# Kernel tuning notes

Hardware: AMD Instinct MI355X
Metric: run time of the kernel (lower is better)

Reference implementation:

```python
import jax, jax.numpy as jnp
import numpy as np

F = 64          # n_features
H = F * F       # n_hidden = 4096
P = 4           # proj_size
T = 8192        # timesteps


def _proj_lstm_cell_zero_state(x, W_ih, W_hh, b_ih, b_hh, W_hr):
    """One PyTorch proj-LSTM layer applied per-timestep with zero initial
    (h, c). x: [T, in_dim] -> [T, P].  With h0=0, W_hh contributes 0 and
    f*c_prev vanishes."""
    h0 = jnp.zeros((x.shape[0], W_hh.shape[1]), x.dtype)
    gates = x @ W_ih.T + h0 @ W_hh.T + b_ih + b_hh          # [T, 4H]
    i, f, g, o = jnp.split(gates, 4, axis=-1)               # PyTorch gate order
    c = jax.nn.sigmoid(i) * jnp.tanh(g)                     # f*c0 = 0
    h = jax.nn.sigmoid(o) * jnp.tanh(c)                     # [T, H]
    return h @ W_hr.T                                       # [T, P]


def setup_inputs() -> dict:
    key = jax.random.key(0)
    ks = jax.random.split(key, 17)
    s = 0.05
    d = {"x": jax.random.normal(ks[0], (T, F), jnp.float32)}
    shapes = {
        "W_ih_0": (4 * H, F), "W_hh_0": (4 * H, P), "b_ih_0": (4 * H,),
        "b_hh_0": (4 * H,), "W_hr_0": (P, H),
        "W_ih_1": (4 * H, P), "W_hh_1": (4 * H, P), "b_ih_1": (4 * H,),
        "b_hh_1": (4 * H,), "W_hr_1": (P, H),
        "W_ih_2": (4 * H, P), "W_hh_2": (4 * H, P), "b_ih_2": (4 * H,),
        "b_hh_2": (4 * H,), "W_hr_2": (P, H),
    }
    for i, (name, shp) in enumerate(shapes.items()):
        d[name] = s * jax.random.normal(ks[i + 1], shp, jnp.float32)
    return d


def reference(x,
              W_ih_0, W_hh_0, b_ih_0, b_hh_0, W_hr_0,
              W_ih_1, W_hh_1, b_ih_1, b_hh_1, W_hr_1,
              W_ih_2, W_hh_2, b_ih_2, b_hh_2, W_hr_2):
    # study(): inputs.split(1, dim=0) feeds each timestep as a fresh length-1
    # sequence with zero initial state, so timesteps are independent ->
    # vectorize over T instead of the per-step Python loop.
    h = _proj_lstm_cell_zero_state(x, W_ih_0, W_hh_0, b_ih_0, b_hh_0, W_hr_0)
    h = _proj_lstm_cell_zero_state(h, W_ih_1, W_hh_1, b_ih_1, b_hh_1, W_hr_1)
    h = _proj_lstm_cell_zero_state(h, W_ih_2, W_hh_2, b_ih_2, b_hh_2, W_hr_2)
    return h  # [T, P]
```

## Files before the change

### kernel.cpp

```cpp
#include <hip/hip_runtime.h>

#define TSTEPS 8192
#define HDIM 4096
#define PDIM 4
#define KDIM 64

typedef unsigned short u16;
typedef __attribute__((ext_vector_type(8))) short short8;
typedef __attribute__((ext_vector_type(4))) float f32x4;

#define S1 -1.44269504089f
#define S2 -2.88539008177f

#if __has_builtin(__builtin_amdgcn_exp2f)
#define EXP2(x) __builtin_amdgcn_exp2f(x)
#else
#define EXP2(x) exp2f(x)
#endif
__device__ __forceinline__ float rcpf(float x) { return __builtin_amdgcn_rcpf(x); }

__device__ __forceinline__ float h_merge(float c, float ec) {
  float c2 = c * c;
  float num = c * fmaf(c2, 10.0f, 105.0f);
  float den = fmaf(c2, 45.0f, 105.0f) + c2 * c2;
  return num * rcpf(den * (1.0f + ec));
}

__device__ __forceinline__ float sig_poly(float z) {
  float z2 = z * z;
  float q = fmaf(z2, -2.1081349e-4f, 2.0833333e-3f);
  q = fmaf(z2, q, -2.0833333e-2f);
  q = fmaf(z2, q, 0.25f);
  return fmaf(z, q, 0.5f);
}
__device__ __forceinline__ float tanh_poly(float z) {
  float z2 = z * z;
  float q = fmaf(z2, -5.3968254e-2f, 1.3333333e-1f);
  q = fmaf(z2, q, -3.3333333e-1f);
  q = fmaf(z2, q, 1.0f);
  return z * q;
}

__device__ __forceinline__ void gload16(const void* g, void* l) {
  __builtin_amdgcn_global_load_lds((const __attribute__((address_space(1))) unsigned int*)g,
                                   (__attribute__((address_space(3))) unsigned int*)l,
                                   16, 0, 0);
}

__device__ __forceinline__ u16 bf16_rne(float f) {
  unsigned u = __float_as_uint(f);
  u += 0x7FFF + ((u >> 16) & 1);
  return (u16)(u >> 16);
}
__device__ __forceinline__ void hilo(float v, u16& h, u16& l) {
  h = bf16_rne(v);
  l = bf16_rne(v - __uint_as_float((unsigned)h << 16));
}

#define WS_Y0   0
#define WS_Y1   32768
#define WS_BSC  65536
#define WS_C1   77824
#define WS_C2   159744
#define WS_XHI  241664
#define WS_XLO  503808
#define WS_WHI  765952
#define WS_WLO  1159168
#define WS_PP   1552384
#define WS_BP   3649536

__global__ void prep_kernel(const float* __restrict__ x,
                            const float* __restrict__ Wih0, const float* __restrict__ bih0,
                            const float* __restrict__ bhh0,
                            const float* __restrict__ Wih1, const float* __restrict__ bih1,
                            const float* __restrict__ bhh1, const float* __restrict__ Whr1,
                            const float* __restrict__ Wih2, const float* __restrict__ bih2,
                            const float* __restrict__ bhh2, const float* __restrict__ Whr2,
                            float* __restrict__ ws) {
  const int i = blockIdx.x * 256 + threadIdx.x;
  u16* xhi = (u16*)(ws + WS_XHI);
  u16* xlo = (u16*)(ws + WS_XLO);
  u16* whi = (u16*)(ws + WS_WHI);
  u16* wlo = (u16*)(ws + WS_WLO);

  if (i < 131072) {
    float4 v = *(const float4*)&x[i * 4];
    float val[4] = {v.x, v.y, v.z, v.w};
    u16 h[4], l[4];
#pragma unroll
    for (int e = 0; e < 4; ++e) hilo(val[e], h[e], l[e]);
    *(ushort4*)&xhi[i * 4] = make_ushort4(h[0], h[1], h[2], h[3]);
    *(ushort4*)&xlo[i * 4] = make_ushort4(l[0], l[1], l[2], l[3]);
  } else if (i < 327680) {
    int f = i - 131072;
    int el4 = f * 4;
    int r = el4 >> 6;
    int k4 = el4 & 63;
    int gate = r >> 12, jr = r & 4095;
    int src = (gate == 0) ? jr : (gate + 1) * HDIM + jr;
    float sc = (gate == 1) ? S2 : S1;
    float4 v = *(const float4*)&Wih0[(size_t)src * KDIM + k4];
    float val[4] = {sc * v.x, sc * v.y, sc * v.z, sc * v.w};
    u16 h[4], l[4];
#pragma unroll
    for (int e = 0; e < 4; ++e) hilo(val[e], h[e], l[e]);
    *(ushort4*)&whi[r * KDIM + k4] = make_ushort4(h[0], h[1], h[2], h[3]);
    *(ushort4*)&wlo[r * KDIM + k4] = make_ushort4(l[0], l[1], l[2], l[3]);
  } else if (i < 339968) {
    int f = i - 327680;
    int g = f >> 12, j = f & 4095;
    int src = (g == 0) ? j : (g + 1) * HDIM + j;
    float sc = (g == 1) ? S2 : S1;
    ws[WS_BSC + f] = sc * (bih0[src] + bhh0[src]);
  } else if (i < 348160) {
    int f = i - 339968;
    const float* Wih = (f < 4096) ? Wih1 : Wih2;
    const float* bih = (f < 4096) ? bih1 : bih2;
    const float* bhh = (f < 4096) ? bhh1 : bhh2;
    const float* Whr = (f < 4096) ? Whr1 : Whr2;
    float* c = ws + ((f < 4096) ? WS_C1 : WS_C2);
    int j = f & 4095;
    *(float4*)(c + j * 4)         = *(const float4*)&Wih[(size_t)j * 4];
    *(float4*)(c + 16384 + j * 4) = *(const float4*)&Wih[(size_t)(2 * HDIM + j) * 4];
    *(float4*)(c + 32768 + j * 4) = *(const float4*)&Wih[(size_t)(3 * HDIM + j) * 4];
    *(float4*)(c + 49152 + j * 4) = make_float4(bih[j] + bhh[j],
                                      bih[2 * HDIM + j] + bhh[2 * HDIM + j],
                                      bih[3 * HDIM + j] + bhh[3 * HDIM + j], 0.f);
    *(float4*)(c + 65536 + j * 4) = make_float4(Whr[j], Whr[HDIM + j], Whr[2 * HDIM + j], Whr[3 * HDIM + j]);
  } else if (i < 446464) {
    int f = i - 348160;
    int lane = f & 63;
    int tg = f >> 6;
    int L = tg / 768;
    int r2 = tg - L * 768;
    int g = r2 >> 8, tile = r2 & 255;
    const float* Wih = (L == 0) ? Wih1 : Wih2;
    const float* bih = (L == 0) ? bih1 : bih2;
    const float* bhh = (L == 0) ? bhh1 : bhh2;
    int q = lane >> 4, n = lane & 15;
    int j = tile * 16 + n;
    int go = (g == 0) ? 0 : (g + 1) * HDIM;
    u16 v[8] = {0, 0, 0, 0, 0, 0, 0, 0};
    if (q < 2) {
#pragma unroll
      for (int e = 0; e < 8; ++e) {
        float wv = Wih[(size_t)(go + j) * 4 + (e & 3)];
        u16 h, l;
        hilo(wv, h, l);
        v[e] = (q == 0) ? h : l;
      }
    } else if (q == 2) {
      float bv = bih[go + j] + bhh[go + j];
      hilo(bv, v[0], v[1]);
    }
    u16* bpp = (u16*)(ws + WS_BP);
    *(short8*)&bpp[(size_t)f * 8] =
        (short8){(short)v[0], (short)v[1], (short)v[2], (short)v[3],
                 (short)v[4], (short)v[5], (short)v[6], (short)v[7]};
  }
}

__global__ __launch_bounds__(256, 2)
void lstm_layer0_mfma(const u16* __restrict__ xhi, const u16* __restrict__ xlo,
                      const u16* __restrict__ whi, const u16* __restrict__ wlo,
                      const float* __restrict__ bsc, const float* __restrict__ Whr,
                      float* __restrict__ pp) {
  __shared__ __align__(16) char smem[65536];
  u16* lw_hi = (u16*)smem;
  u16* lw_lo = (u16*)(smem + 24576);
  u16* lx    = (u16*)(smem + 49152);

  const int tid = threadIdx.x;
  const int w = tid >> 6, lane = tid & 63;
  const int m = lane & 15, q = lane >> 4;
  const int jb = blockIdx.x & 63, tbb = blockIdx.x >> 6;
  const int j0 = jb * 64;
  const int t0 = tbb * 256;

  const int r8_ = lane >> 3;
  const int swo = ((lane & 7) ^ r8_) * 8;

#pragma unroll
  for (int ui = 0; ui < 16; ++ui) {
    const int u = w * 16 + ui;
    const u16* g;
    char* l;
    if (u < 24) {
      g = whi + (size_t)((u >> 3) * HDIM + j0 + (u & 7) * 8 + r8_) * 64 + swo;
      l = smem + u * 1024;
    } else if (u < 48) {
      int uu = u - 24;
      g = wlo + (size_t)((uu >> 3) * HDIM + j0 + (uu & 7) * 8 + r8_) * 64 + swo;
      l = smem + 24576 + uu * 1024;
    } else {
      int uu = u - 48;
      g = xhi + (size_t)(t0 + uu * 8 + r8_) * 64 + swo;
      l = smem + 49152 + uu * 1024;
    }
    gload16(g, l);
  }

  float whr_v[4][4];
#pragma unroll
  for (int p = 0; p < 4; ++p)
#pragma unroll
    for (int js = 0; js < 4; ++js)
      whr_v[p][js] = Whr[(size_t)p * HDIM + j0 + js * 16 + m];
  float biv[4], bgv[4], bov[4];
#pragma unroll
  for (int js = 0; js < 4; ++js) {
    const int j = j0 + js * 16 + m;
    biv[js] = bsc[j];
    bgv[js] = bsc[HDIM + j];
    bov[js] = bsc[2 * HDIM + j];
  }

  f32x4 acc[2][4][3];
  short8 al[2][2];

  auto zero_acc = [&]() {
#pragma unroll
    for (int ts = 0; ts < 2; ++ts)
#pragma unroll
      for (int js = 0; js < 4; ++js)
#pragma unroll
        for (int g = 0; g < 3; ++g) acc[ts][js][g] = (f32x4){0.f, 0.f, 0.f, 0.f};
  };
  auto load_al = [&](int tt) {
#pragma unroll
    for (int kc = 0; kc < 2; ++kc)
#pragma unroll
      for (int ts = 0; ts < 2; ++ts)
        al[kc][ts] = *(const short8*)&xlo[(size_t)(t0 + tt * 128 + w * 32 + ts * 16 + m) * KDIM + kc * 32 + q * 8];
  };
  auto compute = [&]() {
#pragma unroll
    for (int kc = 0; kc < 2; ++kc) {
      const int cs = ((kc * 4 + q) ^ (m & 7)) * 8;
      short8 ah[2];
#pragma unroll
      for (int ts = 0; ts < 2; ++ts)
        ah[ts] = *(const short8*)&lx[(w * 32 + ts * 16 + m) * 64 + cs];
#pragma unroll
      for (int js = 0; js < 4; ++js) {
#pragma unroll
        for (int g = 0; g < 3; ++g) {
          const int roff = (g * 64 + js * 16 + m) * 64 + cs;
          short8 bh = *(const short8*)&lw_hi[roff];
          short8 bl = *(const short8*)&lw_lo[roff];
#pragma unroll
          for (int ts = 0; ts < 2; ++ts) {
            acc[ts][js][g] = __builtin_amdgcn_mfma_f32_16x16x32_bf16(ah[ts], bh, acc[ts][js][g], 0, 0, 0);
            acc[ts][js][g] = __builtin_amdgcn_mfma_f32_16x16x32_bf16(al[kc][ts], bh, acc[ts][js][g], 0, 0, 0);
            acc[ts][js][g] = __builtin_amdgcn_mfma_f32_16x16x32_bf16(ah[ts], bl, acc[ts][js][g], 0, 0, 0);
          }
        }
      }
    }
  };
  auto act_proj = [&](int tt) {
    float hreg[2][4][4];
#pragma unroll
    for (int js = 0; js < 4; ++js) {
#pragma unroll
      for (int ts = 0; ts < 2; ++ts) {
#pragma unroll
        for (int r = 0; r < 4; ++r) {
          float ea = EXP2(acc[ts][js][0][r] + biv[js]);
          float eb = EXP2(acc[ts][js][1][r] + bgv[js]);
          float c = (1.0f - eb) * rcpf((1.0f + ea) * (1.0f + eb));
          float ec = EXP2(acc[ts][js][2][r] + bov[js]);
          hreg[ts][js][r] = h_merge(c, ec);
        }
      }
    }
#pragma unroll
    for (int ts = 0; ts < 2; ++ts) {
#pragma unroll
      for (int r = 0; r < 4; ++r) {
        float pv[4];
#pragma unroll
        for (int p = 0; p < 4; ++p) {
          float s = 0.f;
#pragma unroll
          for (int js = 0; js < 4; ++js) s = fmaf(hreg[ts][js][r], whr_v[p][js], s);
#pragma unroll
          for (int ofs = 1; ofs < 16; ofs <<= 1) s += __shfl_xor(s, ofs, 16);
          pv[p] = s;
        }
        if (m == 0) {
          const int t = t0 + tt * 128 + w * 32 + ts * 16 + q * 4 + r;
          *(float4*)&pp[((size_t)jb * TSTEPS + t) * PDIM] = make_float4(pv[0], pv[1], pv[2], pv[3]);
        }
      }
    }
  };

  load_al(0);
  zero_acc();
  __syncthreads();
  compute();
  __syncthreads();
#pragma unroll
  for (int ui = 0; ui < 4; ++ui) {
    const int u = w * 4 + ui;
    gload16(xhi + (size_t)(t0 + 128 + u * 8 + r8_) * 64 + swo, smem + 49152 + u * 1024);
  }
  load_al(1);
  act_proj(0);
  zero_acc();
  __syncthreads();
  compute();
  act_proj(1);
}

__global__ void fused_rest(const float* __restrict__ pp,
                           const float* __restrict__ c1, const float* __restrict__ c2,
                           const u16* __restrict__ bp,
                           float* __restrict__ out) {
  __shared__ float ytile[64];
  __shared__ float part[256];
  const int tid = threadIdx.x;
  const int t0 = blockIdx.x * 16;
  const int lane = tid & 63, w = tid >> 6;
  const int n = lane & 15, q = lane >> 4;

  {
    const int o = tid & 63;
    const int sg = tid >> 6;
    float s = 0.f;
#pragma unroll 4
    for (int k = sg * 16; k < sg * 16 + 16; ++k)
      s += pp[(size_t)k * (TSTEPS * PDIM) + t0 * PDIM + o];
    part[sg * 64 + o] = s;
  }
  __syncthreads();
  if (tid < 64) ytile[tid] = part[tid] + part[64 + tid] + part[128 + tid] + part[192 + tid];
  __syncthreads();

#pragma unroll
  for (int L = 0; L < 2; ++L) {
    const float4* cwr = (const float4*)(((L == 0) ? c1 : c2) + 65536);
    const u16* bL = bp + (size_t)L * 393216;

    float4 yv = *(const float4*)&ytile[n * 4];
    float ye[4] = {yv.x, yv.y, yv.z, yv.w};
    u16 yh[4], yl[4];
#pragma unroll
    for (int e = 0; e < 4; ++e) hilo(ye[e], yh[e], yl[e]);
    short8 af = (short8){0, 0, 0, 0, 0, 0, 0, 0};
    if (q < 2) {
      af[0] = (short)yh[0]; af[1] = (short)yh[1]; af[2] = (short)yh[2]; af[3] = (short)yh[3];
      af[4] = (short)yl[0]; af[5] = (short)yl[1]; af[6] = (short)yl[2]; af[7] = (short)yl[3];
    } else if (q == 2) {
      af[0] = (short)0x3F80;
      af[1] = (short)0x3F80;
    }

    float o_[4][4];
#pragma unroll
    for (int r = 0; r < 4; ++r)
#pragma unroll
      for (int p = 0; p < 4; ++p) o_[r][p] = 0.f;

#pragma unroll 2
    for (int jt = 0; jt < 64; ++jt) {
      const int tile = w * 64 + jt;
      short8 bfi = *(const short8*)&bL[((size_t)(0 * 256 + tile) * 64 + lane) * 8];
      short8 bfg = *(const short8*)&bL[((size_t)(1 * 256 + tile) * 64 + lane) * 8];
      short8 bfo = *(const short8*)&bL[((size_t)(2 * 256 + tile) * 64 + lane) * 8];
      const f32x4 zc = (f32x4){0.f, 0.f, 0.f, 0.f};
      f32x4 ai = __builtin_amdgcn_mfma_f32_16x16x32_bf16(af, bfi, zc, 0, 0, 0);
      f32x4 ag = __builtin_amdgcn_mfma_f32_16x16x32_bf16(af, bfg, zc, 0, 0, 0);
      f32x4 ao = __builtin_amdgcn_mfma_f32_16x16x32_bf16(af, bfo, zc, 0, 0, 0);
      float4 wr = cwr[tile * 16 + n];
#pragma unroll
      for (int r = 0; r < 4; ++r) {
        float cc = sig_poly(ai[r]) * tanh_poly(ag[r]);
        float h = tanh_poly(cc) * sig_poly(ao[r]);
        o_[r][0] = fmaf(h, wr.x, o_[r][0]);
        o_[r][1] = fmaf(h, wr.y, o_[r][1]);
        o_[r][2] = fmaf(h, wr.z, o_[r][2]);
        o_[r][3] = fmaf(h, wr.w, o_[r][3]);
      }
    }

#pragma unroll
    for (int r = 0; r < 4; ++r)
#pragma unroll
      for (int p = 0; p < 4; ++p) {
#pragma unroll
        for (int ofs = 1; ofs < 16; ofs <<= 1)
          o_[r][p] += __shfl_xor(o_[r][p], ofs, 16);
      }
    __syncthreads();
    if (n == 0) {
#pragma unroll
      for (int r = 0; r < 4; ++r)
#pragma unroll
        for (int p = 0; p < 4; ++p)
          part[w * 64 + (q * 4 + r) * 4 + p] = o_[r][p];
    }
    __syncthreads();
    if (tid < 64) ytile[tid] = part[tid] + part[64 + tid] + part[128 + tid] + part[192 + tid];
    __syncthreads();
  }

  if (tid < 64) out[t0 * PDIM + tid] = ytile[tid];
}

extern "C" void kernel_launch(void* const* d_in, const int* in_sizes, int n_in,
                              void* d_out, int out_size, void* d_ws, size_t ws_size,
                              hipStream_t stream) {
  const float* x    = (const float*)d_in[0];
  const float* Wih0 = (const float*)d_in[1];
  const float* bih0 = (const float*)d_in[3];
  const float* bhh0 = (const float*)d_in[4];
  const float* Whr0 = (const float*)d_in[5];
  const float* Wih1 = (const float*)d_in[6];
  const float* bih1 = (const float*)d_in[8];
  const float* bhh1 = (const float*)d_in[9];
  const float* Whr1 = (const float*)d_in[10];
  const float* Wih2 = (const float*)d_in[11];
  const float* bih2 = (const float*)d_in[13];
  const float* bhh2 = (const float*)d_in[14];
  const float* Whr2 = (const float*)d_in[15];
  float* out = (float*)d_out;
  float* ws = (float*)d_ws;
  float* pp = ws + WS_PP;

  prep_kernel<<<dim3(1744), dim3(256), 0, stream>>>(
      x, Wih0, bih0, bhh0, Wih1, bih1, bhh1, Whr1, Wih2, bih2, bhh2, Whr2, ws);

  lstm_layer0_mfma<<<dim3(2048), dim3(256), 0, stream>>>(
      (const u16*)(ws + WS_XHI), (const u16*)(ws + WS_XLO),
      (const u16*)(ws + WS_WHI), (const u16*)(ws + WS_WLO),
      ws + WS_BSC, Whr0, pp);

  fused_rest<<<dim3(512), dim3(256), 0, stream>>>(
      pp, ws + WS_C1, ws + WS_C2, (const u16*)(ws + WS_BP), out);
}
```

Before: 210.5 us.

## Load x fragments from global into registers and raise layer0 occupancy; widen fused_rest tiles

In layer 0, the x-hi tile is no longer staged in LDS. Its A fragments are loaded straight from global into registers, which cuts shared memory from 64KB to 48KB and lets launch bounds ask for 3 blocks per CU. The mid-kernel syncthreads barriers and LDS refill go away. The Whr load moves into the activation step to ease register pressure, at the cost of more register-held A operands and uncoalesced global reads. fused_rest now uses 512-thread blocks over 32 timesteps, so each weight fragment feeds two MFMA groups and weight traffic per block is halved.

```diff
diff --git a/kernel.cpp b/kernel.cpp
--- a/kernel.cpp
+++ b/kernel.cpp
@@ -160,15 +160,14 @@
   }
 }
 
-__global__ __launch_bounds__(256, 2)
+__global__ __launch_bounds__(256, 3)
 void lstm_layer0_mfma(const u16* __restrict__ xhi, const u16* __restrict__ xlo,
                       const u16* __restrict__ whi, const u16* __restrict__ wlo,
                       const float* __restrict__ bsc, const float* __restrict__ Whr,
                       float* __restrict__ pp) {
-  __shared__ __align__(16) char smem[65536];
+  __shared__ __align__(16) char smem[49152];
   u16* lw_hi = (u16*)smem;
   u16* lw_lo = (u16*)(smem + 24576);
-  u16* lx    = (u16*)(smem + 49152);
 
   const int tid = threadIdx.x;
   const int w = tid >> 6, lane = tid & 63;
@@ -181,31 +180,18 @@
   const int swo = ((lane & 7) ^ r8_) * 8;
 
 #pragma unroll
-  for (int ui = 0; ui < 16; ++ui) {
-    const int u = w * 16 + ui;
+  for (int ui = 0; ui < 12; ++ui) {
+    const int u = w * 12 + ui;
     const u16* g;
-    char* l;
     if (u < 24) {
       g = whi + (size_t)((u >> 3) * HDIM + j0 + (u & 7) * 8 + r8_) * 64 + swo;
-      l = smem + u * 1024;
-    } else if (u < 48) {
-      int uu = u - 24;
+    } else {
+      const int uu = u - 24;
       g = wlo + (size_t)((uu >> 3) * HDIM + j0 + (uu & 7) * 8 + r8_) * 64 + swo;
-      l = smem + 24576 + uu * 1024;
-    } else {
-      int uu = u - 48;
-      g = xhi + (size_t)(t0 + uu * 8 + r8_) * 64 + swo;
-      l = smem + 49152 + uu * 1024;
-    }
-    gload16(g, l);
+    }
+    gload16(g, smem + u * 1024);
   }
 
-  float whr_v[4][4];
-#pragma unroll
-  for (int p = 0; p < 4; ++p)
-#pragma unroll
-    for (int js = 0; js < 4; ++js)
-      whr_v[p][js] = Whr[(size_t)p * HDIM + j0 + js * 16 + m];
   float biv[4], bgv[4], bov[4];
 #pragma unroll
   for (int js = 0; js < 4; ++js) {
@@ -216,7 +202,7 @@
   }
 
   f32x4 acc[2][4][3];
-  short8 al[2][2];
+  short8 ah[2][2], al[2][2];
 
   auto zero_acc = [&]() {
 #pragma unroll
@@ -226,21 +212,20 @@
 #pragma unroll
         for (int g = 0; g < 3; ++g) acc[ts][js][g] = (f32x4){0.f, 0.f, 0.f, 0.f};
   };
-  auto load_al = [&](int tt) {
+  auto load_x = [&](int tt) {
 #pragma unroll
     for (int kc = 0; kc < 2; ++kc)
 #pragma unroll
-      for (int ts = 0; ts < 2; ++ts)
-        al[kc][ts] = *(const short8*)&xlo[(size_t)(t0 + tt * 128 + w * 32 + ts * 16 + m) * KDIM + kc * 32 + q * 8];
+      for (int ts = 0; ts < 2; ++ts) {
+        const size_t off = (size_t)(t0 + tt * 128 + w * 32 + ts * 16 + m) * KDIM + kc * 32 + q * 8;
+        ah[kc][ts] = *(const short8*)&xhi[off];
+        al[kc][ts] = *(const short8*)&xlo[off];
+      }
   };
   auto compute = [&]() {
 #pragma unroll
     for (int kc = 0; kc < 2; ++kc) {
       const int cs = ((kc * 4 + q) ^ (m & 7)) * 8;
-      short8 ah[2];
-#pragma unroll
-      for (int ts = 0; ts < 2; ++ts)
-        ah[ts] = *(const short8*)&lx[(w * 32 + ts * 16 + m) * 64 + cs];
 #pragma unroll
       for (int js = 0; js < 4; ++js) {
 #pragma unroll
@@ -250,32 +235,35 @@
           short8 bl = *(const short8*)&lw_lo[roff];
 #pragma unroll
           for (int ts = 0; ts < 2; ++ts) {
-            acc[ts][js][g] = __builtin_amdgcn_mfma_f32_16x16x32_bf16(ah[ts], bh, acc[ts][js][g], 0, 0, 0);
+            acc[ts][js][g] = __builtin_amdgcn_mfma_f32_16x16x32_bf16(ah[kc][ts], bh, acc[ts][js][g], 0, 0, 0);
             acc[ts][js][g] = __builtin_amdgcn_mfma_f32_16x16x32_bf16(al[kc][ts], bh, acc[ts][js][g], 0, 0, 0);
-            acc[ts][js][g] = __builtin_amdgcn_mfma_f32_16x16x32_bf16(ah[ts], bl, acc[ts][js][g], 0, 0, 0);
+            acc[ts][js][g] = __builtin_amdgcn_mfma_f32_16x16x32_bf16(ah[kc][ts], bl, acc[ts][js][g], 0, 0, 0);
           }
         }
       }
     }
   };
   auto act_proj = [&](int tt) {
-    float hreg[2][4][4];
-#pragma unroll
-    for (int js = 0; js < 4; ++js) {
-#pragma unroll
-      for (int ts = 0; ts < 2; ++ts) {
+    float whr_v[4][4];
+#pragma unroll
+    for (int p = 0; p < 4; ++p)
+#pragma unroll
+      for (int js = 0; js < 4; ++js)
+        whr_v[p][js] = Whr[(size_t)p * HDIM + j0 + js * 16 + m];
+#pragma unroll
+    for (int ts = 0; ts < 2; ++ts) {
+      float hreg[4][4];
+#pragma unroll
+      for (int js = 0; js < 4; ++js) {
 #pragma unroll
         for (int r = 0; r < 4; ++r) {
           float ea = EXP2(acc[ts][js][0][r] + biv[js]);
           float eb = EXP2(acc[ts][js][1][r] + bgv[js]);
           float c = (1.0f - eb) * rcpf((1.0f + ea) * (1.0f + eb));
           float ec = EXP2(acc[ts][js][2][r] + bov[js]);
-          hreg[ts][js][r] = h_merge(c, ec);
-        }
-      }
-    }
-#pragma unroll
-    for (int ts = 0; ts < 2; ++ts) {
+          hreg[js][r] = h_merge(c, ec);
+        }
+      }
 #pragma unroll
       for (int r = 0; r < 4; ++r) {
         float pv[4];
@@ -283,7 +271,7 @@
         for (int p = 0; p < 4; ++p) {
           float s = 0.f;
 #pragma unroll
-          for (int js = 0; js < 4; ++js) s = fmaf(hreg[ts][js][r], whr_v[p][js], s);
+          for (int js = 0; js < 4; ++js) s = fmaf(hreg[js][r], whr_v[p][js], s);
 #pragma unroll
           for (int ofs = 1; ofs < 16; ofs <<= 1) s += __shfl_xor(s, ofs, 16);
           pv[p] = s;
@@ -296,46 +284,42 @@
     }
   };
 
-  load_al(0);
+  load_x(0);
   zero_acc();
   __syncthreads();
   compute();
-  __syncthreads();
-#pragma unroll
-  for (int ui = 0; ui < 4; ++ui) {
-    const int u = w * 4 + ui;
-    gload16(xhi + (size_t)(t0 + 128 + u * 8 + r8_) * 64 + swo, smem + 49152 + u * 1024);
-  }
-  load_al(1);
   act_proj(0);
+  load_x(1);
   zero_acc();
-  __syncthreads();
   compute();
   act_proj(1);
 }
 
-__global__ void fused_rest(const float* __restrict__ pp,
-                           const float* __restrict__ c1, const float* __restrict__ c2,
-                           const u16* __restrict__ bp,
-                           float* __restrict__ out) {
-  __shared__ float ytile[64];
-  __shared__ float part[256];
+__global__ __launch_bounds__(512)
+void fused_rest(const float* __restrict__ pp,
+                const float* __restrict__ c1, const float* __restrict__ c2,
+                const u16* __restrict__ bp,
+                float* __restrict__ out) {
+  __shared__ float ytile[128];
+  __shared__ float part[512];
   const int tid = threadIdx.x;
-  const int t0 = blockIdx.x * 16;
+  const int t0 = blockIdx.x * 32;
   const int lane = tid & 63, w = tid >> 6;
   const int n = lane & 15, q = lane >> 4;
+  const int gt = w >> 2;
+  const int wj = w & 3;
 
   {
-    const int o = tid & 63;
-    const int sg = tid >> 6;
+    const int o = tid & 127;
+    const int sg = tid >> 7;
     float s = 0.f;
 #pragma unroll 4
     for (int k = sg * 16; k < sg * 16 + 16; ++k)
       s += pp[(size_t)k * (TSTEPS * PDIM) + t0 * PDIM + o];
-    part[sg * 64 + o] = s;
+    part[sg * 128 + o] = s;
   }
   __syncthreads();
-  if (tid < 64) ytile[tid] = part[tid] + part[64 + tid] + part[128 + tid] + part[192 + tid];
+  if (tid < 128) ytile[tid] = part[tid] + part[128 + tid] + part[256 + tid] + part[384 + tid];
   __syncthreads();
 
 #pragma unroll
@@ -343,70 +327,88 @@
     const float4* cwr = (const float4*)(((L == 0) ? c1 : c2) + 65536);
     const u16* bL = bp + (size_t)L * 393216;
 
-    float4 yv = *(const float4*)&ytile[n * 4];
-    float ye[4] = {yv.x, yv.y, yv.z, yv.w};
-    u16 yh[4], yl[4];
-#pragma unroll
-    for (int e = 0; e < 4; ++e) hilo(ye[e], yh[e], yl[e]);
-    short8 af = (short8){0, 0, 0, 0, 0, 0, 0, 0};
-    if (q < 2) {
-      af[0] = (short)yh[0]; af[1] = (short)yh[1]; af[2] = (short)yh[2]; af[3] = (short)yh[3];
-      af[4] = (short)yl[0]; af[5] = (short)yl[1]; af[6] = (short)yl[2]; af[7] = (short)yl[3];
-    } else if (q == 2) {
-      af[0] = (short)0x3F80;
-      af[1] = (short)0x3F80;
-    }
-
-    float o_[4][4];
-#pragma unroll
-    for (int r = 0; r < 4; ++r)
-#pragma unroll
-      for (int p = 0; p < 4; ++p) o_[r][p] = 0.f;
+    short8 af[2];
+#pragma unroll
+    for (int g = 0; g < 2; ++g) {
+      float4 yv = *(const float4*)&ytile[g * 64 + n * 4];
+      float ye[4] = {yv.x, yv.y, yv.z, yv.w};
+      u16 yh[4], yl[4];
+#pragma unroll
+      for (int e = 0; e < 4; ++e) hilo(ye[e], yh[e], yl[e]);
+      short8 a = (short8){0, 0, 0, 0, 0, 0, 0, 0};
+      if (q < 2) {
+        a[0] = (short)yh[0]; a[1] = (short)yh[1]; a[2] = (short)yh[2]; a[3] = (short)yh[3];
+        a[4] = (short)yl[0]; a[5] = (short)yl[1]; a[6] = (short)yl[2]; a[7] = (short)yl[3];
+      } else if (q == 2) {
+        a[0] = (short)0x3F80;
+        a[1] = (short)0x3F80;
+      }
+      af[g] = a;
+    }
+
+    float o_[2][4][4];
+#pragma unroll
+    for (int g = 0; g < 2; ++g)
+#pragma unroll
+      for (int r = 0; r < 4; ++r)
+#pragma unroll
+        for (int p = 0; p < 4; ++p) o_[g][r][p] = 0.f;
 
 #pragma unroll 2
     for (int jt = 0; jt < 64; ++jt) {
-      const int tile = w * 64 + jt;
+      const int tile = wj * 64 + jt;
       short8 bfi = *(const short8*)&bL[((size_t)(0 * 256 + tile) * 64 + lane) * 8];
       short8 bfg = *(const short8*)&bL[((size_t)(1 * 256 + tile) * 64 + lane) * 8];
       short8 bfo = *(const short8*)&bL[((size_t)(2 * 256 + tile) * 64 + lane) * 8];
+      float4 wr = cwr[tile * 16 + n];
       const f32x4 zc = (f32x4){0.f, 0.f, 0.f, 0.f};
-      f32x4 ai = __builtin_amdgcn_mfma_f32_16x16x32_bf16(af, bfi, zc, 0, 0, 0);
-      f32x4 ag = __builtin_amdgcn_mfma_f32_16x16x32_bf16(af, bfg, zc, 0, 0, 0);
-      f32x4 ao = __builtin_amdgcn_mfma_f32_16x16x32_bf16(af, bfo, zc, 0, 0, 0);
-      float4 wr = cwr[tile * 16 + n];
-#pragma unroll
-      for (int r = 0; r < 4; ++r) {
-        float cc = sig_poly(ai[r]) * tanh_poly(ag[r]);
-        float h = tanh_poly(cc) * sig_poly(ao[r]);
-        o_[r][0] = fmaf(h, wr.x, o_[r][0]);
-        o_[r][1] = fmaf(h, wr.y, o_[r][1]);
-        o_[r][2] = fmaf(h, wr.z, o_[r][2]);
-        o_[r][3] = fmaf(h, wr.w, o_[r][3]);
-      }
-    }
-
-#pragma unroll
-    for (int r = 0; r < 4; ++r)
-#pragma unroll
-      for (int p = 0; p < 4; ++p) {
-#pragma unroll
-        for (int ofs = 1; ofs < 16; ofs <<= 1)
-          o_[r][p] += __shfl_xor(o_[r][p], ofs, 16);
-      }
+#pragma unroll
+      for (int g = 0; g < 2; ++g) {
+        f32x4 ai = __builtin_amdgcn_mfma_f32_16x16x32_bf16(af[g], bfi, zc, 0, 0, 0);
+        f32x4 ag = __builtin_amdgcn_mfma_f32_16x16x32_bf16(af[g], bfg, zc, 0, 0, 0);
+        f32x4 ao = __builtin_amdgcn_mfma_f32_16x16x32_bf16(af[g], bfo, zc, 0, 0, 0);
+#pragma unroll
+        for (int r = 0; r < 4; ++r) {
+          float cc = sig_poly(ai[r]) * tanh_poly(ag[r]);
+          float h = tanh_poly(cc) * sig_poly(ao[r]);
+          o_[g][r][0] = fmaf(h, wr.x, o_[g][r][0]);
+          o_[g][r][1] = fmaf(h, wr.y, o_[g][r][1]);
+          o_[g][r][2] = fmaf(h, wr.z, o_[g][r][2]);
+          o_[g][r][3] = fmaf(h, wr.w, o_[g][r][3]);
+        }
+      }
+    }
+
+#pragma unroll
+    for (int g = 0; g < 2; ++g)
+#pragma unroll
+      for (int r = 0; r < 4; ++r)
+#pragma unroll
+        for (int p = 0; p < 4; ++p) {
+#pragma unroll
+          for (int ofs = 1; ofs < 16; ofs <<= 1)
+            o_[g][r][p] += __shfl_xor(o_[g][r][p], ofs, 16);
+        }
     __syncthreads();
     if (n == 0) {
 #pragma unroll
-      for (int r = 0; r < 4; ++r)
-#pragma unroll
-        for (int p = 0; p < 4; ++p)
-          part[w * 64 + (q * 4 + r) * 4 + p] = o_[r][p];
+      for (int g = 0; g < 2; ++g)
+#pragma unroll
+        for (int r = 0; r < 4; ++r)
+#pragma unroll
+          for (int p = 0; p < 4; ++p)
+            part[g * 256 + wj * 64 + (q * 4 + r) * 4 + p] = o_[g][r][p];
     }
     __syncthreads();
-    if (tid < 64) ytile[tid] = part[tid] + part[64 + tid] + part[128 + tid] + part[192 + tid];
+    if (tid < 128) {
+      const int g = tid >> 6, idx = tid & 63;
+      ytile[tid] = part[g * 256 + idx] + part[g * 256 + 64 + idx] +
+                   part[g * 256 + 128 + idx] + part[g * 256 + 192 + idx];
+    }
     __syncthreads();
   }
 
-  if (tid < 64) out[t0 * PDIM + tid] = ytile[tid];
+  if (tid < 128) out[t0 * PDIM + tid] = ytile[tid];
 }
 
 extern "C" void kernel_launch(void* const* d_in, const int* in_sizes, int n_in,
@@ -437,6 +439,6 @@
       (const u16*)(ws + WS_WHI), (const u16*)(ws + WS_WLO),
       ws + WS_BSC, Whr0, pp);
 
-  fused_rest<<<dim3(512), dim3(256), 0, stream>>>(
+  fused_rest<<<dim3(256), dim3(512), 0, stream>>>(
       pp, ws + WS_C1, ws + WS_C2, (const u16*)(ws + WS_BP), out);
 }
```

Result: slower. 291.4 us (+38.4%).

## Split fused small-layer kernel into hidden-dim-partitioned partial kernels plus reductions

Applied to the files above, without the earlier changes.

Replaces the single fused_rest kernel with separate steps: a y0 reduction kernel, then for each of layers 1 and 2 a partial kernel followed by a combine kernel. Each partial kernel splits the 4096-wide hidden dimension into four quarters across blocks and uses 512-thread blocks covering 32 timesteps. The aim is more parallel blocks and waves than the previous 512 blocks of 256 threads, which had to run the hidden loop serially. The cost is four extra kernel launches and global round-trips for the partial sums, which reuse the pp workspace region.

```diff
diff --git a/kernel.cpp b/kernel.cpp
--- a/kernel.cpp
+++ b/kernel.cpp
@@ -314,99 +314,103 @@
   act_proj(1);
 }
 
-__global__ void fused_rest(const float* __restrict__ pp,
-                           const float* __restrict__ c1, const float* __restrict__ c2,
-                           const u16* __restrict__ bp,
-                           float* __restrict__ out) {
-  __shared__ float ytile[64];
-  __shared__ float part[256];
-  const int tid = threadIdx.x;
-  const int t0 = blockIdx.x * 16;
-  const int lane = tid & 63, w = tid >> 6;
-  const int n = lane & 15, q = lane >> 4;
-
-  {
-    const int o = tid & 63;
-    const int sg = tid >> 6;
-    float s = 0.f;
+__global__ void y0_reduce(const float* __restrict__ pp, float* __restrict__ y0) {
+  const int i = blockIdx.x * 256 + threadIdx.x;
+  float s[4];
+#pragma unroll
+  for (int sg = 0; sg < 4; ++sg) {
+    float t = 0.f;
 #pragma unroll 4
     for (int k = sg * 16; k < sg * 16 + 16; ++k)
-      s += pp[(size_t)k * (TSTEPS * PDIM) + t0 * PDIM + o];
-    part[sg * 64 + o] = s;
+      t += pp[(size_t)k * (TSTEPS * PDIM) + i];
+    s[sg] = t;
+  }
+  y0[i] = ((s[0] + s[1]) + s[2]) + s[3];
+}
+
+__global__ void yp_combine(const float* __restrict__ yp, float* __restrict__ yout) {
+  const int i = blockIdx.x * 256 + threadIdx.x;
+  yout[i] = ((yp[i] + yp[32768 + i]) + yp[65536 + i]) + yp[98304 + i];
+}
+
+__global__ __launch_bounds__(512)
+void lstm_small_partial(const float* __restrict__ yin, const u16* __restrict__ bL,
+                        const float* __restrict__ cwr4, float* __restrict__ yp) {
+  __shared__ float part[512];
+  const int tid = threadIdx.x;
+  const int lane = tid & 63, w = tid >> 6;
+  const int n = lane & 15, qq = lane >> 4;
+  const int gt = w >> 2;
+  const int ws_ = w & 3;
+  const int tc = blockIdx.x & 255;
+  const int jq = blockIdx.x >> 8;
+  const int t0 = tc * 32 + gt * 16;
+  const float4* cwr = (const float4*)cwr4;
+
+  float4 yv = *(const float4*)&yin[(size_t)(t0 + n) * 4];
+  float ye[4] = {yv.x, yv.y, yv.z, yv.w};
+  u16 yh[4], yl[4];
+#pragma unroll
+  for (int e = 0; e < 4; ++e) hilo(ye[e], yh[e], yl[e]);
+  short8 af = (short8){0, 0, 0, 0, 0, 0, 0, 0};
+  if (qq < 2) {
+    af[0] = (short)yh[0]; af[1] = (short)yh[1]; af[2] = (short)yh[2]; af[3] = (short)yh[3];
+    af[4] = (short)yl[0]; af[5] = (short)yl[1]; af[6] = (short)yl[2]; af[7] = (short)yl[3];
+  } else if (qq == 2) {
+    af[0] = (short)0x3F80;
+    af[1] = (short)0x3F80;
+  }
+
+  float o_[4][4];
+#pragma unroll
+  for (int r = 0; r < 4; ++r)
+#pragma unroll
+    for (int p = 0; p < 4; ++p) o_[r][p] = 0.f;
+
+#pragma unroll 4
+  for (int jt = 0; jt < 16; ++jt) {
+    const int tile = jq * 64 + ws_ * 16 + jt;
+    short8 bfi = *(const short8*)&bL[((size_t)(0 * 256 + tile) * 64 + lane) * 8];
+    short8 bfg = *(const short8*)&bL[((size_t)(1 * 256 + tile) * 64 + lane) * 8];
+    short8 bfo = *(const short8*)&bL[((size_t)(2 * 256 + tile) * 64 + lane) * 8];
+    float4 wr = cwr[tile * 16 + n];
+    const f32x4 zc = (f32x4){0.f, 0.f, 0.f, 0.f};
+    f32x4 ai = __builtin_amdgcn_mfma_f32_16x16x32_bf16(af, bfi, zc, 0, 0, 0);
+    f32x4 ag = __builtin_amdgcn_mfma_f32_16x16x32_bf16(af, bfg, zc, 0, 0, 0);
+    f32x4 ao = __builtin_amdgcn_mfma_f32_16x16x32_bf16(af, bfo, zc, 0, 0, 0);
+#pragma unroll
+    for (int r = 0; r < 4; ++r) {
+      float cc = sig_poly(ai[r]) * tanh_poly(ag[r]);
+      float h = tanh_poly(cc) * sig_poly(ao[r]);
+      o_[r][0] = fmaf(h, wr.x, o_[r][0]);
+      o_[r][1] = fmaf(h, wr.y, o_[r][1]);
+      o_[r][2] = fmaf(h, wr.z, o_[r][2]);
+      o_[r][3] = fmaf(h, wr.w, o_[r][3]);
+    }
+  }
+
+#pragma unroll
+  for (int r = 0; r < 4; ++r)
+#pragma unroll
+    for (int p = 0; p < 4; ++p) {
+#pragma unroll
+      for (int ofs = 1; ofs < 16; ofs <<= 1)
+        o_[r][p] += __shfl_xor(o_[r][p], ofs, 16);
+    }
+  if (n == 0) {
+#pragma unroll
+    for (int r = 0; r < 4; ++r)
+#pragma unroll
+      for (int p = 0; p < 4; ++p)
+        part[gt * 256 + ws_ * 64 + (qq * 4 + r) * 4 + p] = o_[r][p];
   }
   __syncthreads();
-  if (tid < 64) ytile[tid] = part[tid] + part[64 + tid] + part[128 + tid] + part[192 + tid];
-  __syncthreads();
-
-#pragma unroll
-  for (int L = 0; L < 2; ++L) {
-    const float4* cwr = (const float4*)(((L == 0) ? c1 : c2) + 65536);
-    const u16* bL = bp + (size_t)L * 393216;
-
-    float4 yv = *(const float4*)&ytile[n * 4];
-    float ye[4] = {yv.x, yv.y, yv.z, yv.w};
-    u16 yh[4], yl[4];
-#pragma unroll
-    for (int e = 0; e < 4; ++e) hilo(ye[e], yh[e], yl[e]);
-    short8 af = (short8){0, 0, 0, 0, 0, 0, 0, 0};
-    if (q < 2) {
-      af[0] = (short)yh[0]; af[1] = (short)yh[1]; af[2] = (short)yh[2]; af[3] = (short)yh[3];
-      af[4] = (short)yl[0]; af[5] = (short)yl[1]; af[6] = (short)yl[2]; af[7] = (short)yl[3];
-    } else if (q == 2) {
-      af[0] = (short)0x3F80;
-      af[1] = (short)0x3F80;
-    }
-
-    float o_[4][4];
-#pragma unroll
-    for (int r = 0; r < 4; ++r)
-#pragma unroll
-      for (int p = 0; p < 4; ++p) o_[r][p] = 0.f;
-
-#pragma unroll 2
-    for (int jt = 0; jt < 64; ++jt) {
-      const int tile = w * 64 + jt;
-      short8 bfi = *(const short8*)&bL[((size_t)(0 * 256 + tile) * 64 + lane) * 8];
-      short8 bfg = *(const short8*)&bL[((size_t)(1 * 256 + tile) * 64 + lane) * 8];
-      short8 bfo = *(const short8*)&bL[((size_t)(2 * 256 + tile) * 64 + lane) * 8];
-      const f32x4 zc = (f32x4){0.f, 0.f, 0.f, 0.f};
-      f32x4 ai = __builtin_amdgcn_mfma_f32_16x16x32_bf16(af, bfi, zc, 0, 0, 0);
-      f32x4 ag = __builtin_amdgcn_mfma_f32_16x16x32_bf16(af, bfg, zc, 0, 0, 0);
-      f32x4 ao = __builtin_amdgcn_mfma_f32_16x16x32_bf16(af, bfo, zc, 0, 0, 0);
-      float4 wr = cwr[tile * 16 + n];
-#pragma unroll
-      for (int r = 0; r < 4; ++r) {
-        float cc = sig_poly(ai[r]) * tanh_poly(ag[r]);
-        float h = tanh_poly(cc) * sig_poly(ao[r]);
-        o_[r][0] = fmaf(h, wr.x, o_[r][0]);
-        o_[r][1] = fmaf(h, wr.y, o_[r][1]);
-        o_[r][2] = fmaf(h, wr.z, o_[r][2]);
-        o_[r][3] = fmaf(h, wr.w, o_[r][3]);
-      }
-    }
-
-#pragma unroll
-    for (int r = 0; r < 4; ++r)
-#pragma unroll
-      for (int p = 0; p < 4; ++p) {
-#pragma unroll
-        for (int ofs = 1; ofs < 16; ofs <<= 1)
-          o_[r][p] += __shfl_xor(o_[r][p], ofs, 16);
-      }
-    __syncthreads();
-    if (n == 0) {
-#pragma unroll
-      for (int r = 0; r < 4; ++r)
-#pragma unroll
-        for (int p = 0; p < 4; ++p)
-          part[w * 64 + (q * 4 + r) * 4 + p] = o_[r][p];
-    }
-    __syncthreads();
-    if (tid < 64) ytile[tid] = part[tid] + part[64 + tid] + part[128 + tid] + part[192 + tid];
-    __syncthreads();
-  }
-
-  if (tid < 64) out[t0 * PDIM + tid] = ytile[tid];
+  if (tid < 128) {
+    const int g2 = tid >> 6, idx = tid & 63;
+    float s = part[g2 * 256 + idx] + part[g2 * 256 + 64 + idx] +
+              part[g2 * 256 + 128 + idx] + part[g2 * 256 + 192 + idx];
+    yp[(size_t)jq * 32768 + (size_t)tc * 128 + tid] = s;
+  }
 }
 
 extern "C" void kernel_launch(void* const* d_in, const int* in_sizes, int n_in,
@@ -428,6 +432,8 @@
   float* out = (float*)d_out;
   float* ws = (float*)d_ws;
   float* pp = ws + WS_PP;
+  float* yp = ws + WS_PP;
+  const u16* bp = (const u16*)(ws + WS_BP);
 
   prep_kernel<<<dim3(1744), dim3(256), 0, stream>>>(
       x, Wih0, bih0, bhh0, Wih1, bih1, bhh1, Whr1, Wih2, bih2, bhh2, Whr2, ws);
@@ -437,6 +443,13 @@
       (const u16*)(ws + WS_WHI), (const u16*)(ws + WS_WLO),
       ws + WS_BSC, Whr0, pp);
 
-  fused_rest<<<dim3(512), dim3(256), 0, stream>>>(
-      pp, ws + WS_C1, ws + WS_C2, (const u16*)(ws + WS_BP), out);
-}
+  y0_reduce<<<dim3(128), dim3(256), 0, stream>>>(pp, ws + WS_Y0);
+
+  lstm_small_partial<<<dim3(1024), dim3(512), 0, stream>>>(
+      ws + WS_Y0, bp, ws + WS_C1 + 65536, yp);
+  yp_combine<<<dim3(128), dim3(256), 0, stream>>>(yp, ws + WS_Y1);
+
+  lstm_small_partial<<<dim3(1024), dim3(512), 0, stream>>>(
+      ws + WS_Y1, bp + 393216, ws + WS_C2 + 65536, yp);
+  yp_combine<<<dim3(128), dim3(256), 0, stream>>>(yp, out);
+}
```

After: 216.6 us. +2.9%, slower.
